# Kernel tuning notes

Measured on AMD Instinct MI355X. Metric: run time of the kernel, lower is better.

Reference implementation:

```python
import jax, jax.numpy as jnp
import numpy as np

# LIF / memristor constants (from AnalogNeuron and ResistiveMemoryElement defaults)
T, B, N, M = 1024, 16, 2048, 512
DT = 1e-7            # simulation timestep (s)
CMEM = 1e-12         # membrane capacitance (F)
G_LEAK = 1e-9        # leak conductance (S)
VTH = 0.7            # threshold voltage (V)
VRESET = 0.0         # reset voltage
REFRAC = 1e-6        # refractory period (s) -> 10 steps
TAU_ADAPT = 1e-4     # adaptation time constant (s)
ADAPT_INC = 5e-11    # adaptation current increment on spike (A)
GAIN = 1.0           # gain_mismatch
OFFSET = 0.0         # offset_voltage
I_NOISE_STD = 1e-12  # current_noise std (A)
V_NOISE_STD = 1e-3   # voltage_noise std (V)
READ_V = 0.1         # memristor read voltage (V)
MAX_R = 1e8          # max resistance -> min conductance clip
COND_NOISE_STD = 0.1118  # sqrt(0.1^2 + 0.05^2): device variation + read noise, relative
EXT_SCALE = 1e-6     # external drive scale (A): dV/step ~ 0.1 V


def setup_inputs() -> dict:
    key = jax.random.key(0)
    k1, k2, k3, k4, k5 = jax.random.split(key, 5)
    ext_current = jax.random.normal(k1, (T, B, N), dtype=jnp.float32) * EXT_SCALE
    i_noise = jax.random.normal(k2, (T, B, N), dtype=jnp.float32) * I_NOISE_STD
    v_noise = jax.random.normal(k3, (T, B, N), dtype=jnp.float32) * V_NOISE_STD
    # conductances of a 2048x512 RRAM crossbar: resistances 1e5..1e7 ohm -> G in [1e-7, 1e-5] S
    G = jax.random.uniform(k4, (N, M), dtype=jnp.float32, minval=1e-7, maxval=1e-5)
    cond_noise = jax.random.normal(k5, (N, M), dtype=jnp.float32)
    return {"ext_current": ext_current, "i_noise": i_noise, "v_noise": v_noise,
            "G": G, "cond_noise": cond_noise}


def reference(ext_current, i_noise, v_noise, G, cond_noise):
    dtype = ext_current.dtype
    t_steps = ext_current.shape[0]
    t_arr = jnp.arange(t_steps, dtype=dtype) * DT  # wall-clock time per step

    def step(carry, xs):
        V, A, last_spike = carry          # [B,N] each
        ext, inz, vnz, t = xs
        active = (t - last_spike) >= REFRAC
        total_I = ext - A + inz           # excitatory - adaptation + noise current
        Vn = V + DT * (total_I - G_LEAK * V) / CMEM + vnz + OFFSET
        An = A * (1.0 - DT / TAU_ADAPT)   # A += dt*(-A/tau)
        V1 = jnp.where(active, Vn, V)
        A1 = jnp.where(active, An, A)
        spike = active & (V1 >= VTH * GAIN)
        V2 = jnp.where(spike, VRESET, V1)
        A2 = jnp.where(spike, A1 + ADAPT_INC, A1)
        ls2 = jnp.where(spike, t, last_spike)
        return (V2, A2, ls2), spike.astype(dtype)

    V0 = jnp.zeros(ext_current.shape[1:], dtype)
    A0 = jnp.zeros_like(V0)
    ls0 = jnp.full_like(V0, -1e9)  # last_spike_time = -inf
    (Vf, Af, _), spikes = jax.lax.scan(step, (V0, A0, ls0),
                                       (ext_current, i_noise, v_noise, t_arr))
    rates = spikes.mean(axis=0)  # [B,N] firing rates
    # memristive crossbar read: noisy conductance, clipped at 1/max_R, read at READ_V
    Gn = jnp.maximum(1.0 / MAX_R, G * (1.0 + COND_NOISE_STD * cond_noise))
    readout = rates @ (Gn * READ_V)  # [B,M]
    return readout
```

## Files before the change

kernel.cpp:

```cpp
#include <hip/hip_runtime.h>

namespace {

constexpr int T_STEPS = 1024;
constexpr int BATCH   = 16;
constexpr int NNEUR   = 2048;
constexpr int MCOLS   = 512;
constexpr int BN      = BATCH * NNEUR;

constexpr double DT_D   = 1e-7;
constexpr double TAU_D  = 1e-4;

constexpr float DT_F     = 1e-7f;
constexpr float CMEM_F   = 1e-12f;
constexpr float GLEAK_F  = 1e-9f;
constexpr float VTH_F    = 0.7f;
constexpr float REFRAC_F = 1e-6f;
constexpr float AINC_F   = 5e-11f;
constexpr float DECAY_F  = (float)(1.0 - DT_D / TAU_D);
constexpr float VRESET_F = 0.0f;

constexpr int NPB     = 128;
constexpr int C_STEPS = 8;
constexpr int NBUF    = T_STEPS / C_STEPS;
constexpr int RING    = 6;
constexpr int AHEAD   = 4;
constexpr int IPW     = 12;
constexpr size_t BUF_STRIDE = (size_t)C_STEPS * BN;

}

#define LIF_STEP(ec, ic, vc, tidx)                                         \
    do {                                                                   \
        float t      = (float)(tidx) * DT_F;                               \
        bool  active = (t - ls) >= REFRAC_F;                               \
        float totI   = ((ec) - A) + (ic);                                  \
        float Vn     = (V + (DT_F * (totI - GLEAK_F * V)) / CMEM_F) + (vc);\
        float An     = A * DECAY_F;                                        \
        float V1     = active ? Vn : V;                                    \
        float A1     = active ? An : A;                                    \
        bool  spike  = active && (V1 >= VTH_F);                            \
        V  = spike ? VRESET_F : V1;                                        \
        A  = spike ? (A1 + AINC_F) : A1;                                   \
        ls = spike ? t : ls;                                               \
        count += spike ? 1 : 0;                                            \
    } while (0)

__global__ __launch_bounds__(384, 1) void lif_sim_kernel(
    const float* __restrict__ ext,
    const float* __restrict__ inz,
    const float* __restrict__ vnz,
    float* __restrict__ rates)
{
    __shared__ float slotmem[RING][3][C_STEPS][NPB];

    const int tid  = threadIdx.x;
    const int lane = tid & 63;
    const int w    = tid >> 6;
    const int n0   = blockIdx.x * NPB;

    if (w >= 2) {
        const int lw = w - 2;
        const float* pg[IPW];
        int loff[IPW];
#pragma unroll
        for (int i = 0; i < IPW; ++i) {
            const int idx = lw * IPW + i;
            const int r   = idx >> 1;
            const int h   = idx & 1;
            const int a   = r >> 3;
            const int tt  = r & 7;
            const float* ba = (a == 0) ? ext : ((a == 1) ? inz : vnz);
            pg[i]   = ba + (size_t)tt * BN + (n0 + h * 64 + lane);
            loff[i] = (a * C_STEPS + tt) * NPB + h * 64;
        }

        float* const slot0 = &slotmem[0][0][0][0];
        constexpr int SLOT_F = 3 * C_STEPS * NPB;

        auto issue = [&](int j) {
            float* sb = slot0 + (j % RING) * SLOT_F;
#pragma unroll
            for (int i = 0; i < IPW; ++i) {
                __builtin_amdgcn_global_load_lds(
                    (const __attribute__((address_space(1))) void*)
                        (pg[i] + (size_t)j * BUF_STRIDE),
                    (__attribute__((address_space(3))) void*)(sb + loff[i]),
                    4, 0, 0);
            }
        };

        for (int j = 0; j < AHEAD; ++j) issue(j);

        for (int k = 0; k < NBUF; ++k) {
            const int rem = NBUF - 1 - k;
            const int nb  = (rem < AHEAD - 1) ? rem : (AHEAD - 1);
            switch (nb) {
                case 3:  asm volatile("s_waitcnt vmcnt(36)" ::: "memory"); break;
                case 2:  asm volatile("s_waitcnt vmcnt(24)" ::: "memory"); break;
                case 1:  asm volatile("s_waitcnt vmcnt(12)" ::: "memory"); break;
                default: asm volatile("s_waitcnt vmcnt(0)"  ::: "memory"); break;
            }
            __builtin_amdgcn_sched_barrier(0);
            __builtin_amdgcn_s_barrier();
            __builtin_amdgcn_sched_barrier(0);
            if (k + AHEAD < NBUF) issue(k + AHEAD);
        }
    } else {
        float V = 0.0f, A = 0.0f, ls = -1e9f;
        int count = 0;

        for (int k = 0; k < NBUF; ++k) {
            __builtin_amdgcn_s_barrier();
            __builtin_amdgcn_sched_barrier(0);
            const int s = k % RING;
#pragma unroll
            for (int c = 0; c < C_STEPS; ++c) {
                float ec = slotmem[s][0][c][tid];
                float ic = slotmem[s][1][c][tid];
                float vc = slotmem[s][2][c][tid];
                LIF_STEP(ec, ic, vc, k * C_STEPS + c);
            }
            __builtin_amdgcn_sched_barrier(0);
        }
        rates[n0 + tid] = (float)count * (1.0f / 1024.0f);
    }
}

constexpr int KC   = 8;
constexpr int KCH  = NNEUR / KC;
constexpr int KSUB = 4;
constexpr int KPT  = KCH / KSUB;

__global__ __launch_bounds__(256) void readout_partial_kernel(
    const float* __restrict__ rates,
    const float* __restrict__ G,
    const float* __restrict__ cn,
    float* __restrict__ part)
{
    __shared__ float red[KSUB][64][BATCH + 1];

    const int tid = threadIdx.x;
    const int ml  = tid & 63;
    const int s   = tid >> 6;
    const int m   = blockIdx.x * 64 + ml;
    const int kc  = blockIdx.y;
    const int k0  = kc * KCH + s * KPT;

    float acc[BATCH];
#pragma unroll
    for (int b = 0; b < BATCH; ++b) acc[b] = 0.0f;

#pragma unroll 4
    for (int k = k0; k < k0 + KPT; ++k) {
        float g = G[(size_t)k * MCOLS + m];
        float c = cn[(size_t)k * MCOLS + m];
        float w = fmaxf(1e-8f, g * (1.0f + 0.1118f * c)) * 0.1f;
#pragma unroll
        for (int b = 0; b < BATCH; ++b) {
            acc[b] = fmaf(rates[b * NNEUR + k], w, acc[b]);
        }
    }

#pragma unroll
    for (int b = 0; b < BATCH; ++b) red[s][ml][b] = acc[b];
    __syncthreads();

    if (s == 0) {
#pragma unroll
        for (int b = 0; b < BATCH; ++b) {
            float v = ((red[0][ml][b] + red[1][ml][b]) + red[2][ml][b]) + red[3][ml][b];
            part[((size_t)kc * BATCH + b) * MCOLS + m] = v;
        }
    }
}

__global__ __launch_bounds__(256) void readout_reduce_kernel(
    const float* __restrict__ part,
    float* __restrict__ out)
{
    const int i = blockIdx.x * 256 + threadIdx.x;
    float s = 0.0f;
#pragma unroll
    for (int kc = 0; kc < KC; ++kc) {
        s += part[kc * (BATCH * MCOLS) + i];
    }
    out[i] = s;
}

extern "C" void kernel_launch(void* const* d_in, const int* in_sizes, int n_in,
                              void* d_out, int out_size, void* d_ws, size_t ws_size,
                              hipStream_t stream)
{
    const float* ext = (const float*)d_in[0];
    const float* inz = (const float*)d_in[1];
    const float* vnz = (const float*)d_in[2];
    const float* G   = (const float*)d_in[3];
    const float* cn  = (const float*)d_in[4];
    float* out = (float*)d_out;

    float* rates = (float*)d_ws;
    float* part  = rates + BN;

    lif_sim_kernel<<<BN / NPB, 384, 0, stream>>>(ext, inz, vnz, rates);
    readout_partial_kernel<<<dim3(MCOLS / 64, KC), 256, 0, stream>>>(rates, G, cn, part);
    readout_reduce_kernel<<<(BATCH * MCOLS) / 256, 256, 0, stream>>>(part, out);
}
```

Before: 113.1 us.

## Replace LDS-direct loads with float4 register double-buffer using eight loader waves

The loader path moves from per-float global_load_lds into a six-slot ring to 16-byte float4 loads staged in registers and written to a two-slot LDS double buffer. The block grows to eight loader waves plus two compute waves, and the chunk size doubles to 16 steps, halving the number of barriers. The aim is wider memory transactions and more loads in flight per CU. In exchange, prefetch depth drops to two chunks, loaded data takes an extra trip through registers, and LDS writes and their waits now sit on the loader waves.

```diff
diff --git a/kernel.cpp b/kernel.cpp
--- a/kernel.cpp
+++ b/kernel.cpp
@@ -21,11 +21,10 @@
 constexpr float VRESET_F = 0.0f;
 
 constexpr int NPB     = 128;
-constexpr int C_STEPS = 8;
+constexpr int C_STEPS = 16;
 constexpr int NBUF    = T_STEPS / C_STEPS;
-constexpr int RING    = 6;
-constexpr int AHEAD   = 4;
-constexpr int IPW     = 12;
+constexpr int LWAVES  = 8;
+constexpr int FPW     = 3;
 constexpr size_t BUF_STRIDE = (size_t)C_STEPS * BN;
 
 }
@@ -46,84 +45,94 @@
         count += spike ? 1 : 0;                                            \
     } while (0)
 
-__global__ __launch_bounds__(384, 1) void lif_sim_kernel(
+__global__ __launch_bounds__(640, 1) void lif_sim_kernel(
     const float* __restrict__ ext,
     const float* __restrict__ inz,
     const float* __restrict__ vnz,
     float* __restrict__ rates)
 {
-    __shared__ float slotmem[RING][3][C_STEPS][NPB];
+    __shared__ float smem[2][3][C_STEPS][NPB];
 
     const int tid  = threadIdx.x;
     const int lane = tid & 63;
     const int w    = tid >> 6;
     const int n0   = blockIdx.x * NPB;
 
-    if (w >= 2) {
-        const int lw = w - 2;
-        const float* pg[IPW];
-        int loff[IPW];
-#pragma unroll
-        for (int i = 0; i < IPW; ++i) {
-            const int idx = lw * IPW + i;
-            const int r   = idx >> 1;
-            const int h   = idx & 1;
-            const int a   = r >> 3;
-            const int tt  = r & 7;
+    if (w < LWAVES) {
+        const float* gp[FPW];
+        float* d0[FPW];
+        float* d1[FPW];
+#pragma unroll
+        for (int i = 0; i < FPW; ++i) {
+            const int e  = i * 512 + w * 64 + lane;
+            const int a  = e >> 9;
+            const int ea = e & 511;
+            const int tt = ea >> 5;
+            const int n4 = (ea & 31) * 4;
             const float* ba = (a == 0) ? ext : ((a == 1) ? inz : vnz);
-            pg[i]   = ba + (size_t)tt * BN + (n0 + h * 64 + lane);
-            loff[i] = (a * C_STEPS + tt) * NPB + h * 64;
-        }
-
-        float* const slot0 = &slotmem[0][0][0][0];
-        constexpr int SLOT_F = 3 * C_STEPS * NPB;
-
-        auto issue = [&](int j) {
-            float* sb = slot0 + (j % RING) * SLOT_F;
-#pragma unroll
-            for (int i = 0; i < IPW; ++i) {
-                __builtin_amdgcn_global_load_lds(
-                    (const __attribute__((address_space(1))) void*)
-                        (pg[i] + (size_t)j * BUF_STRIDE),
-                    (__attribute__((address_space(3))) void*)(sb + loff[i]),
-                    4, 0, 0);
+            gp[i] = ba + (size_t)tt * BN + (n0 + n4);
+            d0[i] = &smem[0][a][tt][n4];
+            d1[i] = &smem[1][a][tt][n4];
+        }
+
+        float4 ra[FPW], rb[FPW];
+
+#define ISSUE(R)                                                           \
+        do {                                                               \
+            _Pragma("unroll")                                              \
+            for (int i = 0; i < FPW; ++i) {                                \
+                R[i] = *(const float4*)gp[i];                              \
+                gp[i] += BUF_STRIDE;                                       \
+            }                                                              \
+        } while (0)
+
+        ISSUE(ra); ISSUE(rb);
+
+        for (int j = 0; j < NBUF; j += 2) {
+            asm volatile("s_waitcnt vmcnt(3)" ::: "memory");
+            __builtin_amdgcn_sched_barrier(0);
+#pragma unroll
+            for (int i = 0; i < FPW; ++i) *(float4*)d0[i] = ra[i];
+            asm volatile("s_waitcnt lgkmcnt(0)" ::: "memory");
+            if (j + 2 < NBUF) { ISSUE(ra); }
+            __builtin_amdgcn_sched_barrier(0);
+            __builtin_amdgcn_s_barrier();
+            __builtin_amdgcn_sched_barrier(0);
+
+            if (j + 1 < NBUF - 1) {
+                asm volatile("s_waitcnt vmcnt(3)" ::: "memory");
+            } else {
+                asm volatile("s_waitcnt vmcnt(0)" ::: "memory");
             }
-        };
-
-        for (int j = 0; j < AHEAD; ++j) issue(j);
-
-        for (int k = 0; k < NBUF; ++k) {
-            const int rem = NBUF - 1 - k;
-            const int nb  = (rem < AHEAD - 1) ? rem : (AHEAD - 1);
-            switch (nb) {
-                case 3:  asm volatile("s_waitcnt vmcnt(36)" ::: "memory"); break;
-                case 2:  asm volatile("s_waitcnt vmcnt(24)" ::: "memory"); break;
-                case 1:  asm volatile("s_waitcnt vmcnt(12)" ::: "memory"); break;
-                default: asm volatile("s_waitcnt vmcnt(0)"  ::: "memory"); break;
-            }
+            __builtin_amdgcn_sched_barrier(0);
+#pragma unroll
+            for (int i = 0; i < FPW; ++i) *(float4*)d1[i] = rb[i];
+            asm volatile("s_waitcnt lgkmcnt(0)" ::: "memory");
+            if (j + 3 < NBUF) { ISSUE(rb); }
             __builtin_amdgcn_sched_barrier(0);
             __builtin_amdgcn_s_barrier();
             __builtin_amdgcn_sched_barrier(0);
-            if (k + AHEAD < NBUF) issue(k + AHEAD);
-        }
+        }
+#undef ISSUE
     } else {
+        const int tc = tid - LWAVES * 64;
         float V = 0.0f, A = 0.0f, ls = -1e9f;
         int count = 0;
 
         for (int k = 0; k < NBUF; ++k) {
             __builtin_amdgcn_s_barrier();
             __builtin_amdgcn_sched_barrier(0);
-            const int s = k % RING;
+            const int s = k & 1;
 #pragma unroll
             for (int c = 0; c < C_STEPS; ++c) {
-                float ec = slotmem[s][0][c][tid];
-                float ic = slotmem[s][1][c][tid];
-                float vc = slotmem[s][2][c][tid];
+                float ec = smem[s][0][c][tc];
+                float ic = smem[s][1][c][tc];
+                float vc = smem[s][2][c][tc];
                 LIF_STEP(ec, ic, vc, k * C_STEPS + c);
             }
             __builtin_amdgcn_sched_barrier(0);
         }
-        rates[n0 + tid] = (float)count * (1.0f / 1024.0f);
+        rates[n0 + tc] = (float)count * (1.0f / 1024.0f);
     }
 }
 
@@ -202,7 +211,7 @@
     float* rates = (float*)d_ws;
     float* part  = rates + BN;
 
-    lif_sim_kernel<<<BN / NPB, 384, 0, stream>>>(ext, inz, vnz, rates);
+    lif_sim_kernel<<<BN / NPB, 640, 0, stream>>>(ext, inz, vnz, rates);
     readout_partial_kernel<<<dim3(MCOLS / 64, KC), 256, 0, stream>>>(rates, G, cn, part);
     readout_reduce_kernel<<<(BATCH * MCOLS) / 256, 256, 0, stream>>>(part, out);
 }
```

New measurement: 167.8 us. 48.3% more time.
